# Optimization experiments

Hardware: AMD Instinct MI355X
Metric: run time of the kernel (lower is better)

Reference implementation:

```python
import jax, jax.numpy as jnp
import numpy as np

B, NW, NS, SL = 32, 500, 50, 40
EMB, HID, VOCAB, E = 300, 150, 50000, 563200
N = B * (NW + NS)
MAXPOS = 512


def _sinusoid(n_pos, d):
    pos = np.arange(n_pos)[:, None].astype(np.float64)
    i = np.arange(d)[None, :]
    ang = pos / np.power(10000.0, 2 * (i // 2) / d)
    tab = np.zeros((n_pos, d))
    tab[:, 0::2] = np.sin(ang[:, 0::2])
    tab[:, 1::2] = np.cos(ang[:, 1::2])
    tab[0] = 0.0  # padding_idx=0
    return jnp.asarray(tab, dtype=jnp.float32)

_POS_TAB = _sinusoid(MAXPOS + 1, EMB)


def setup_inputs():
    keys = iter(jax.random.split(jax.random.key(0), 48))
    def nrm(shape, s=0.05):
        return jax.random.normal(next(keys), shape, dtype=jnp.float32) * s
    inp = {}
    inp["x"] = jax.random.randint(next(keys), (B, NW), 0, VOCAB, dtype=jnp.int32)
    inp["sent_x"] = jax.random.randint(next(keys), (B, NS, SL), 0, VOCAB, dtype=jnp.int32)
    inp["edge_index"] = jax.random.randint(next(keys), (2, E), 0, N, dtype=jnp.int32)
    inp["embed_table"] = nrm((VOCAB, EMB)).at[0].set(0.0)  # padding_idx=0
    for h in range(2, 8):
        inp["conv_w%d" % h] = nrm((50, 1, h, EMB))
        inp["conv_b%d" % h] = nrm((50,))
    inp["cnn_proj_w"] = nrm((HID, EMB)); inp["cnn_proj_b"] = nrm((HID,))
    inp["lstm_w_ih_l0"] = nrm((2, 4 * HID, HID)); inp["lstm_w_hh_l0"] = nrm((2, 4 * HID, HID))
    inp["lstm_b_ih_l0"] = nrm((2, 4 * HID)); inp["lstm_b_hh_l0"] = nrm((2, 4 * HID))
    inp["lstm_w_ih_l1"] = nrm((2, 4 * HID, 2 * HID)); inp["lstm_w_hh_l1"] = nrm((2, 4 * HID, HID))
    inp["lstm_b_ih_l1"] = nrm((2, 4 * HID)); inp["lstm_b_hh_l1"] = nrm((2, 4 * HID))
    inp["lstm_proj_w"] = nrm((HID, 2 * HID)); inp["lstm_proj_b"] = nrm((HID,))
    inp["gc0_w"] = nrm((HID, EMB)); inp["gc0_b"] = nrm((HID,))
    inp["gc1_w"] = nrm((HID, HID)); inp["gc1_b"] = nrm((HID,))
    inp["gc2_w"] = nrm((HID, HID)); inp["gc2_b"] = nrm((HID,))
    return inp


def _forward(x, sent_x, edge_index, embed_table, conv_ws, conv_bs,
             cnn_proj_w, cnn_proj_b, w_ih0, w_hh0, b_ih0, b_hh0,
             w_ih1, w_hh1, b_ih1, b_hh1, lstm_proj_w, lstm_proj_b,
             gc0_w, gc0_b, gc1_w, gc1_b, gc2_w, gc2_b):
    Bsz, S, L = sent_x.shape
    Nn = Bsz * S
    emb_words = embed_table[x]                                   # [B, NW, EMB]
    tok = embed_table[sent_x].reshape(Nn, L, EMB)                # [Nn, L, EMB]
    sentlen = (sent_x != 0).sum(-1).reshape(Nn)                  # token count per sentence
    a = jnp.arange(L)
    input_pos = jnp.where(a[None, :] < sentlen[:, None], a[None, :] + 1, 0)
    enc = tok + _POS_TAB[input_pos]
    # CNN ngram features: conv heights 2..7, full-width kernels == windowed matmuls
    feats = []
    for w, b in zip(conv_ws, conv_bs):
        h = w.shape[2]
        acc = b + sum(jnp.einsum('nld,od->nlo', enc[:, k:L - h + 1 + k, :], w[:, 0, k, :]) for k in range(h))
        feats.append(jnp.max(jax.nn.relu(acc), axis=1))          # [Nn, 50]
    ngram = jnp.concatenate(feats, axis=1)                        # [Nn, 300]
    snode_pos = jnp.tile(jnp.arange(S), Bsz)
    cnn_feat = ((ngram + _POS_TAB[snode_pos]) @ cnn_proj_w.T + cnn_proj_b).reshape(Bsz, S, HID)
    glen = (sent_x[:, :, 0] != 0).sum(-1)                         # valid sentence count per graph

    def lstm_dir(xs, w_ih, w_hh, bias):
        def step(carry, xt):
            hh, cc = carry
            g = xt @ w_ih.T + hh @ w_hh.T + bias
            i, f, gg, o = jnp.split(g, 4, axis=-1)
            cc = jax.nn.sigmoid(f) * cc + jax.nn.sigmoid(i) * jnp.tanh(gg)
            hh = jax.nn.sigmoid(o) * jnp.tanh(cc)
            return (hh, cc), hh
        z = jnp.zeros((xs.shape[0], HID), xs.dtype)
        _, hs = jax.lax.scan(step, (z, z), jnp.swapaxes(xs, 0, 1))
        return jnp.swapaxes(hs, 0, 1)

    def rev_within(xs):
        # reverse only the first glen[b] steps (packed-sequence semantics)
        T = xs.shape[1]; t = jnp.arange(T)
        idx = jnp.where(t[None, :] < glen[:, None], glen[:, None] - 1 - t[None, :], t[None, :])
        return jnp.take_along_axis(xs, idx[:, :, None], axis=1)

    def bidir(xs, w_ih, w_hh, b_i, b_h):
        f = lstm_dir(xs, w_ih[0], w_hh[0], b_i[0] + b_h[0])
        r = rev_within(lstm_dir(rev_within(xs), w_ih[1], w_hh[1], b_i[1] + b_h[1]))
        return jnp.concatenate([f, r], axis=-1)

    h1 = bidir(cnn_feat, w_ih0, w_hh0, b_ih0, b_hh0)
    h2 = bidir(h1, w_ih1, w_hh1, b_ih1, b_hh1)
    mask = (jnp.arange(S)[None, :] < glen[:, None]).astype(h2.dtype)[:, :, None]
    lstm_feat = (h2 * mask) @ lstm_proj_w.T + lstm_proj_b
    sent_out = jnp.concatenate([cnn_feat, lstm_feat], axis=-1)    # [B, S, 300]
    nodes = jnp.concatenate([emb_words, sent_out], axis=1)        # [B, NW+S, 300]
    nodes = (nodes @ gc0_w.T + gc0_b).reshape(-1, HID)            # [N, 150]
    Nt = nodes.shape[0]
    loop = jnp.arange(Nt, dtype=edge_index.dtype)
    src = jnp.concatenate([edge_index[0], loop])                  # add self-loops
    dst = jnp.concatenate([edge_index[1], loop])
    deg = jax.ops.segment_sum(jnp.ones(src.shape[0], nodes.dtype), dst, num_segments=Nt)
    dis = jnp.where(deg > 0, jax.lax.rsqrt(deg), 0.0)
    norm = (dis[src] * dis[dst])[:, None]

    def gcn(xin, w, bias):
        xw = xin @ w.T
        return jax.ops.segment_sum(xw[src] * norm, dst, num_segments=Nt) + bias

    h = jax.nn.elu(gcn(nodes, gc1_w, gc1_b))
    # F.dropout with training=False -> identity
    return gcn(h, gc2_w, gc2_b), emb_words


def reference(x, sent_x, edge_index, embed_table, conv_w2, conv_b2, conv_w3, conv_b3,
              conv_w4, conv_b4, conv_w5, conv_b5, conv_w6, conv_b6, conv_w7, conv_b7,
              cnn_proj_w, cnn_proj_b, lstm_w_ih_l0, lstm_w_hh_l0, lstm_b_ih_l0, lstm_b_hh_l0,
              lstm_w_ih_l1, lstm_w_hh_l1, lstm_b_ih_l1, lstm_b_hh_l1, lstm_proj_w, lstm_proj_b,
              gc0_w, gc0_b, gc1_w, gc1_b, gc2_w, gc2_b):
    conv_ws = [conv_w2, conv_w3, conv_w4, conv_w5, conv_w6, conv_w7]
    conv_bs = [conv_b2, conv_b3, conv_b4, conv_b5, conv_b6, conv_b7]
    return _forward(x, sent_x, edge_index, embed_table, conv_ws, conv_bs,
                    cnn_proj_w, cnn_proj_b, lstm_w_ih_l0, lstm_w_hh_l0, lstm_b_ih_l0, lstm_b_hh_l0,
                    lstm_w_ih_l1, lstm_w_hh_l1, lstm_b_ih_l1, lstm_b_hh_l1, lstm_proj_w, lstm_proj_b,
                    gc0_w, gc0_b, gc1_w, gc1_b, gc2_w, gc2_b)
```

## Files before the change

kernel.cpp:

```cpp
#include <hip/hip_runtime.h>
#include <stdint.h>
#include <math.h>

#define EDGES 563200
#define NNODES 17600
#define OUT0SZ 2640000
#define MROWS 64000
#define MPAD  64016
#define KSTRIDE 2112

typedef _Float16 h2 __attribute__((ext_vector_type(2)));
typedef _Float16 h4 __attribute__((ext_vector_type(4)));
typedef _Float16 v8h __attribute__((ext_vector_type(8)));
typedef float v4f __attribute__((ext_vector_type(4)));

__device__ __forceinline__ float sigm(float x){ return 1.f / (1.f + expf(-x)); }

__device__ __forceinline__ float fdot2_(h2 a, h2 b, float c){
#if __has_builtin(__builtin_amdgcn_fdot2)
  return __builtin_amdgcn_fdot2(a, b, c, false);
#else
  return c + (float)a.x * (float)b.x + (float)a.y * (float)b.y;
#endif
}

__device__ __forceinline__ void stage16(const char* g, char* lds_base, int lane){
#if __has_builtin(__builtin_amdgcn_global_load_lds)
  __builtin_amdgcn_global_load_lds(
      (const __attribute__((address_space(1))) void*)g,
      (__attribute__((address_space(3))) void*)lds_base, 16, 0, 0);
#else
  uint4 v = *(const uint4*)g;
  *(uint4*)(lds_base + lane * 16) = v;
#endif
}

__global__ void gcnk_postab(float* __restrict__ pos){
  int idx = blockIdx.x * 256 + threadIdx.x;
  if (idx >= 513 * 300) return;
  int p = idx / 300, i = idx - p * 300;
  float v = 0.f;
  if (p != 0){
    double expo = (double)(2 * (i / 2)) / 300.0;
    double ang = (double)p / pow(10000.0, expo);
    v = (float)((i & 1) ? cos(ang) : sin(ang));
  }
  pos[idx] = v;
}

__global__ void gcnk_prep(const int* __restrict__ sx, int* __restrict__ sentlen,
                          int* __restrict__ glen){
  int tid = blockIdx.x * 256 + threadIdx.x;
  if (tid < 1600){
    int c = 0;
    for (int j = 0; j < 40; j++) c += (sx[tid * 40 + j] != 0);
    sentlen[tid] = c;
  } else if (tid < 1632){
    int b = tid - 1600, c = 0;
    for (int s = 0; s < 50; s++) c += (sx[b * 2000 + s * 40] != 0);
    glen[b] = c;
  }
}

__global__ void gcnk_rowmap(const int* __restrict__ glen, int* __restrict__ rowmap){
  int i = blockIdx.x * 256 + threadIdx.x;
  if (i >= 1600) return;
  int b = i / 50, t = i - b * 50, g = glen[b];
  rowmap[i] = b * 50 + ((t < g) ? (g - 1 - t) : t);
}

__global__ void gcnk_embw(const int* __restrict__ x, const float* __restrict__ tab,
                          float4* __restrict__ out){
  int idx = blockIdx.x * 256 + threadIdx.x;
  if (idx >= 16000 * 75) return;
  int row = idx / 75, q = idx - row * 75;
  const float4* t = (const float4*)tab;
  out[idx] = t[x[row] * 75 + q];
}

__global__ void gcnk_zeroi(unsigned int* __restrict__ p, int n){
  int i = blockIdx.x * 256 + threadIdx.x;
  if (i < n) p[i] = 0u;
}

__global__ void gcnk_ench(const int* __restrict__ sx, const float* __restrict__ tab,
                          const float* __restrict__ pos, const int* __restrict__ sentlen,
                          _Float16* __restrict__ ench){
  int idx = blockIdx.x * 256 + threadIdx.x;
  if (idx >= MPAD * 75) return;
  int row = idx / 75, q = idx - row * 75;
  int d = q * 4;
  h4 o; o[0] = (_Float16)0.f; o[1] = (_Float16)0.f; o[2] = (_Float16)0.f; o[3] = (_Float16)0.f;
  if (row < MROWS){
    int n = row / 40, l = row - n * 40;
    int tok = sx[n * 40 + l];
    int p = (l < sentlen[n]) ? (l + 1) : 0;
    float4 a = *(const float4*)(tab + (size_t)tok * 300 + d);
    float4 b = *(const float4*)(pos + (size_t)p * 300 + d);
    o[0] = (_Float16)(a.x + b.x); o[1] = (_Float16)(a.y + b.y);
    o[2] = (_Float16)(a.z + b.z); o[3] = (_Float16)(a.w + b.w);
  }
  *(h4*)(ench + (size_t)row * 300 + d) = o;
}

__global__ void gcnk_bpack(const float* w2, const float* w3, const float* w4,
                           const float* w5, const float* w6, const float* w7,
                           const float* c2, const float* c3, const float* c4,
                           const float* c5, const float* c6, const float* c7,
                           _Float16* __restrict__ Bp, float* __restrict__ bias_p){
  int idx = blockIdx.x * 256 + threadIdx.x;
  if (idx < 2 * 160 * KSTRIDE){
    int n = idx / KSTRIDE, kk = idx - n * KSTRIDE;
    int g = n / 160, c = n - g * 160;
    _Float16 v = (_Float16)0.f;
    if (c < 150){
      int H = 3 * g + 2 + c / 50, o = c % 50;
      if (kk < 300 * H){
        const float* w;
        switch (H){ case 2: w = w2; break; case 3: w = w3; break;
                    case 4: w = w4; break; case 5: w = w5; break;
                    case 6: w = w6; break; default: w = w7; break; }
        v = (_Float16)w[o * 300 * H + kk];
      }
    }
    Bp[idx] = v;
  }
  if (idx < 320){
    int g = idx / 160, c = idx - g * 160;
    float bv = 0.f;
    if (c < 150){
      int H = 3 * g + 2 + c / 50, o = c % 50;
      const float* cbp;
      switch (H){ case 2: cbp = c2; break; case 3: cbp = c3; break;
                  case 4: cbp = c4; break; case 5: cbp = c5; break;
                  case 6: cbp = c6; break; default: cbp = c7; break; }
      bv = cbp[o];
    }
    bias_p[idx] = bv;
  }
}

__global__ __launch_bounds__(256)
void gcnk_convmfma(const _Float16* __restrict__ A, const _Float16* __restrict__ Bp,
                   const float* __restrict__ bias_p, unsigned int* __restrict__ ngram_u){
  __shared__ __align__(1024) char smem[36864];
  _Float16* Asm = (_Float16*)smem;
  _Float16* Bsm = (_Float16*)(smem + 16384);
  float* Cs = (float*)smem;
  const int tid = threadIdx.x;
  const int m0 = blockIdx.x * 128;
  const int grp = blockIdx.y;
  const char* Abase = (const char*)A;
  const char* Bbase = (const char*)(Bp + (size_t)grp * 160 * KSTRIDE);
  const int kmax = grp ? 2112 : 1216;
  const int w = tid >> 6, lane = tid & 63;
  const int wm = (w >> 1) * 64, wn = (w & 1) * 80;
  const int fm = lane & 15, fq = lane >> 4;
  const int lrow = lane >> 3;
  const int loff = (((lane & 7) ^ lrow) << 4);

  v4f acc[4][5] = {};

  for (int kc = 0; kc < kmax; kc += 64){
    #pragma unroll
    for (int ii = 0; ii < 4; ii++){
      int i = w * 4 + ii;
      const char* g = Abase + (size_t)(m0 + i * 8 + lrow) * 600 + kc * 2 + loff;
      stage16(g, (char*)Asm + i * 1024, lane);
    }
    #pragma unroll
    for (int jj = 0; jj < 5; jj++){
      int j = w * 5 + jj;
      const char* g = Bbase + (size_t)(j * 8 + lrow) * (KSTRIDE * 2) + kc * 2 + loff;
      stage16(g, (char*)Bsm + j * 1024, lane);
    }
    __syncthreads();
    #pragma unroll
    for (int ks = 0; ks < 2; ks++){
      const int axor = (ks * 64 + fq * 16) ^ ((fm & 7) << 4);
      v8h af[4], bf[5];
      #pragma unroll
      for (int mt = 0; mt < 4; mt++)
        af[mt] = *(const v8h*)((const char*)Asm + (wm + mt * 16 + fm) * 128 + axor);
      #pragma unroll
      for (int nt = 0; nt < 5; nt++)
        bf[nt] = *(const v8h*)((const char*)Bsm + (wn + nt * 16 + fm) * 128 + axor);
      #pragma unroll
      for (int mt = 0; mt < 4; mt++)
        #pragma unroll
        for (int nt = 0; nt < 5; nt++)
          acc[mt][nt] = __builtin_amdgcn_mfma_f32_16x16x32_f16(af[mt], bf[nt], acc[mt][nt], 0, 0, 0);
    }
    __syncthreads();
  }

  for (int p = 0; p < 5; p++){
    __syncthreads();
    #pragma unroll
    for (int nt = 0; nt < 5; nt++){
      int cstart = wn + nt * 16;
      if ((cstart >> 5) == p){
        int co = cstart - p * 32 + fm;
        #pragma unroll
        for (int mt = 0; mt < 4; mt++)
          #pragma unroll
          for (int r = 0; r < 4; r++)
            Cs[(wm + mt * 16 + fq * 4 + r) * 33 + co] = acc[mt][nt][r];
      }
    }
    __syncthreads();
    if (tid < 128){
      int cl = tid & 31, si = tid >> 5;
      int col = p * 32 + cl;
      if (col < 150){
        int H = 3 * grp + 2 + col / 50, lh = 41 - H;
        int sent = m0 / 40 + si;
        if (sent < 1600){
          int rlo = sent * 40; if (rlo < m0) rlo = m0;
          int rhi = sent * 40 + lh; if (rhi > m0 + 128) rhi = m0 + 128;
          if (rlo < rhi){
            float bv = bias_p[grp * 160 + col];
            float vmax = 0.f;
            for (int r = rlo; r < rhi; r++){
              float v = Cs[(r - m0) * 33 + cl] + bv;
              vmax = fmaxf(vmax, v);
            }
            atomicMax(ngram_u + sent * 300 + grp * 150 + col, __float_as_uint(vmax));
          }
        }
      }
    }
  }
}

__global__ void gcnk_addpos(float* __restrict__ ngram, const float* __restrict__ pos){
  int idx = blockIdx.x * 256 + threadIdx.x;
  if (idx >= 1600 * 300) return;
  int row = idx / 300, d = idx - row * 300;
  ngram[idx] += pos[(row % 50) * 300 + d];
}

template<int BM, int BN, int WMT, int WNT, int OUTH>
__global__ __launch_bounds__(256)
void gcnk_mgemm(const float* __restrict__ A, const float* __restrict__ Wt,
                const float* __restrict__ b1, const float* __restrict__ b2,
                void* __restrict__ Cv, int M, int N, int K){
  __shared__ __align__(16) _Float16 As[BM * 40];
  __shared__ __align__(16) _Float16 Bs[BN * 40];
  const int tid = threadIdx.x;
  const int m0 = blockIdx.x * BM, n0 = blockIdx.y * BN;
  const int w = tid >> 6, lane = tid & 63;
  const int wm = (w >> 1) * (WMT * 16), wn = (w & 1) * (WNT * 16);
  const int fm = lane & 15, fq = lane >> 4;
  v4f acc[WMT][WNT] = {};
  const int nch = (K + 31) >> 5;
  for (int ch = 0; ch < nch; ch++){
    int kc = ch * 32;
    #pragma unroll
    for (int j = 0; j < BM / 64; j++){
      int u = tid + 256 * j;
      int row = u >> 2, cb = (u & 3) * 8;
      int gm = m0 + row, gk = kc + cb;
      v8h vv;
      if (gm < M && gk + 8 <= K){
        const float* p = A + (size_t)gm * K + gk;
        #pragma unroll
        for (int e = 0; e < 8; e++) vv[e] = (_Float16)p[e];
      } else {
        #pragma unroll
        for (int e = 0; e < 8; e++)
          vv[e] = (gm < M && gk + e < K) ? (_Float16)A[(size_t)gm * K + gk + e] : (_Float16)0.f;
      }
      *(v8h*)(As + row * 40 + cb) = vv;
    }
    {
      int row = tid >> 2, cb = (tid & 3) * 8;
      int gn = n0 + row, gk = kc + cb;
      v8h vv;
      if (gn < N && gk + 8 <= K){
        const float* p = Wt + (size_t)gn * K + gk;
        #pragma unroll
        for (int e = 0; e < 8; e++) vv[e] = (_Float16)p[e];
      } else {
        #pragma unroll
        for (int e = 0; e < 8; e++)
          vv[e] = (gn < N && gk + e < K) ? (_Float16)Wt[(size_t)gn * K + gk + e] : (_Float16)0.f;
      }
      *(v8h*)(Bs + row * 40 + cb) = vv;
    }
    __syncthreads();
    v8h af[WMT], bf[WNT];
    #pragma unroll
    for (int mt = 0; mt < WMT; mt++)
      af[mt] = *(const v8h*)(As + (wm + mt * 16 + fm) * 40 + fq * 8);
    #pragma unroll
    for (int nt = 0; nt < WNT; nt++)
      bf[nt] = *(const v8h*)(Bs + (wn + nt * 16 + fm) * 40 + fq * 8);
    #pragma unroll
    for (int mt = 0; mt < WMT; mt++)
      #pragma unroll
      for (int nt = 0; nt < WNT; nt++)
        acc[mt][nt] = __builtin_amdgcn_mfma_f32_16x16x32_f16(af[mt], bf[nt], acc[mt][nt], 0, 0, 0);
    __syncthreads();
  }
  #pragma unroll
  for (int nt = 0; nt < WNT; nt++){
    int gn = n0 + wn + nt * 16 + fm;
    if (gn >= N) continue;
    float badd = (b1 ? b1[gn] : 0.f) + (b2 ? b2[gn] : 0.f);
    #pragma unroll
    for (int mt = 0; mt < WMT; mt++)
      #pragma unroll
      for (int r = 0; r < 4; r++){
        int gm = m0 + wm + mt * 16 + fq * 4 + r;
        if (gm < M){
          float val = acc[mt][nt][r] + badd;
          if (OUTH) ((_Float16*)Cv)[(size_t)gm * 160 + gn] = (_Float16)val;
          else      ((float*)Cv)[(size_t)gm * N + gn] = val;
        }
      }
  }
}

__global__ void gcnk_permute150(float* __restrict__ dst, const float* __restrict__ src,
                                const int* __restrict__ map){
  int idx = blockIdx.x * 256 + threadIdx.x;
  if (idx >= 1600 * 150) return;
  int row = idx / 150, d = idx - row * 150;
  dst[idx] = src[map[row] * 150 + d];
}

__global__ void gcnk_concat(float* __restrict__ dst, const float* __restrict__ A,
                            const float* __restrict__ Bs, const int* __restrict__ mapA,
                            const int* __restrict__ mapB, const int* __restrict__ glen,
                            int usemask){
  int idx = blockIdx.x * 256 + threadIdx.x;
  if (idx >= 1600 * 300) return;
  int row = idx / 300, d = idx - row * 300;
  int b = row / 50, t = row - b * 50;
  float v;
  if (d < 150){ int r = mapA ? mapA[row] : row; v = A[r * 150 + d]; }
  else        { int r = mapB ? mapB[row] : row; v = Bs[r * 150 + d - 150]; }
  if (usemask && t >= glen[b]) v = 0.f;
  dst[idx] = v;
}

__global__ void gcnk_whhpack(const float* __restrict__ whh, _Float16* __restrict__ wpad){
  int idx = blockIdx.x * 256 + threadIdx.x;
  if (idx >= 1200 * 152) return;
  int row = idx / 152, col = idx - row * 152;
  wpad[idx] = (col < 150) ? (_Float16)whh[row * 150 + col] : (_Float16)0.f;
}

__global__ __launch_bounds__(640)
void gcnk_lstm(const float* __restrict__ xf, const float* __restrict__ xr,
               const _Float16* __restrict__ wpad, float* __restrict__ fo,
               float* __restrict__ ro){
  int b = blockIdx.x >> 1, dir = blockIdx.x & 1;
  const float* xih = dir ? xr : xf;
  float* out = dir ? ro : fo;
  __shared__ __align__(16) _Float16 hh[160];
  __shared__ float gates[600];
  const int tid = threadIdx.x;

  h2 w[76];
  if (tid < 600){
    const h2* wrow = (const h2*)(wpad + ((size_t)dir * 600 + tid) * 152);
    #pragma unroll
    for (int j = 0; j < 76; j++) w[j] = wrow[j];
  }
  for (int u = tid; u < 160; u += 640) hh[u] = (_Float16)0.f;
  float creg = 0.f;
  __syncthreads();

  for (int t = 0; t < 50; t++){
    if (tid < 600){
      float acc = xih[(b * 50 + t) * 600 + tid];
      float a0 = 0.f, a1 = 0.f, a2 = 0.f, a3 = 0.f;
      #pragma unroll
      for (int j = 0; j < 19; j++){
        union { float4 f; h2 h[4]; } u;
        u.f = *(const float4*)(hh + j * 8);
        a0 = fdot2_(w[4 * j + 0], u.h[0], a0);
        a1 = fdot2_(w[4 * j + 1], u.h[1], a1);
        a2 = fdot2_(w[4 * j + 2], u.h[2], a2);
        a3 = fdot2_(w[4 * j + 3], u.h[3], a3);
      }
      gates[tid] = acc + ((a0 + a1) + (a2 + a3));
    }
    __syncthreads();
    if (tid < 150){
      float ig = sigm(gates[tid]);
      float fg = sigm(gates[150 + tid]);
      float gg = tanhf(gates[300 + tid]);
      float og = sigm(gates[450 + tid]);
      creg = fg * creg + ig * gg;
      float hn = og * tanhf(creg);
      hh[tid] = (_Float16)hn;
      out[(b * 50 + t) * 150 + tid] = hn;
    }
    __syncthreads();
  }
}

__global__ void gcnk_nodes_in(const int* __restrict__ x, const float* __restrict__ tab,
                              const float* __restrict__ cnnf, const float* __restrict__ lstmf,
                              float* __restrict__ out){
  int idx = blockIdx.x * 256 + threadIdx.x;
  if (idx >= NNODES * 300) return;
  int nrow = idx / 300, d = idx - nrow * 300;
  int b = nrow / 550, j = nrow - b * 550;
  float v;
  if (j < 500) v = tab[x[b * 500 + j] * 300 + d];
  else {
    int r = b * 50 + (j - 500);
    v = (d < 150) ? cnnf[r * 150 + d] : lstmf[r * 150 + d - 150];
  }
  out[idx] = v;
}

__global__ void gcnk_hist(const int* __restrict__ ei, int* __restrict__ ecnt){
  int e = blockIdx.x * 256 + threadIdx.x;
  if (e < EDGES) atomicAdd(&ecnt[ei[EDGES + e]], 1);
}

__global__ __launch_bounds__(1024)
void gcnk_scan(const int* __restrict__ ecnt, int* __restrict__ eoff,
               int* __restrict__ ecur){
  __shared__ int wsum[16];
  int tid = threadIdx.x;
  int base = tid * 18;
  int pre[18];
  int s = 0;
  #pragma unroll
  for (int i = 0; i < 18; i++){
    int idx = base + i;
    int c = (idx < NNODES) ? ecnt[idx] : 0;
    pre[i] = s; s += c;
  }
  int lane = tid & 63, wid = tid >> 6;
  int run = s;
  #pragma unroll
  for (int off = 1; off < 64; off <<= 1){
    int y = __shfl_up(run, off, 64);
    if (lane >= off) run += y;
  }
  if (lane == 63) wsum[wid] = run;
  __syncthreads();
  if (tid == 0){
    int a = 0;
    #pragma unroll
    for (int i = 0; i < 16; i++){ int t2 = wsum[i]; wsum[i] = a; a += t2; }
  }
  __syncthreads();
  int excl = wsum[wid] + run - s;
  #pragma unroll
  for (int i = 0; i < 18; i++){
    int idx = base + i;
    if (idx < NNODES){
      int e = excl + pre[i];
      eoff[idx] = e; ecur[idx] = e;
    }
  }
}

__global__ void gcnk_scatter(const int* __restrict__ ei, int* __restrict__ ecur,
                             int* __restrict__ esrc){
  int e = blockIdx.x * 256 + threadIdx.x;
  if (e < EDGES){
    int d = ei[EDGES + e];
    int p = atomicAdd(&ecur[d], 1);
    esrc[p] = ei[e];
  }
}

__global__ void gcnk_dis2(const int* __restrict__ ecnt, float* __restrict__ dis){
  int i = blockIdx.x * 256 + threadIdx.x;
  if (i < NNODES) dis[i] = rsqrtf((float)(ecnt[i] + 1));
}

__global__ __launch_bounds__(128)
void gcnk_aggcsr_h(const int* __restrict__ eoff, const int* __restrict__ ecnt,
                   const int* __restrict__ esrc, const float* __restrict__ dis,
                   const _Float16* __restrict__ xw, const float* __restrict__ bias,
                   float* __restrict__ out, int doelu){
  int d = blockIdx.x, t = threadIdx.x;
  float dd = dis[d];
  bool act = t < 75;
  float ax = 0.f, ay = 0.f;
  if (act){
    h2 v = *(const h2*)(xw + (size_t)d * 160 + 2 * t);
    ax = (float)v[0] * dd; ay = (float)v[1] * dd;
  }
  int beg = eoff[d], end = beg + ecnt[d];
  for (int j = beg; j < end; j++){
    int s = esrc[j];
    float ds_ = dis[s];
    if (act){
      h2 v = *(const h2*)(xw + (size_t)s * 160 + 2 * t);
      ax += (float)v[0] * ds_; ay += (float)v[1] * ds_;
    }
  }
  if (act){
    float o0 = ax * dd + bias[2 * t];
    float o1 = ay * dd + bias[2 * t + 1];
    if (doelu){
      o0 = (o0 > 0.f) ? o0 : expm1f(o0);
      o1 = (o1 > 0.f) ? o1 : expm1f(o1);
    }
    *(float2*)(out + (size_t)d * 150 + 2 * t) = make_float2(o0, o1);
  }
}

extern "C" void kernel_launch(void* const* d_in, const int* in_sizes, int n_in,
                              void* d_out, int out_size, void* d_ws, size_t ws_size,
                              hipStream_t stream){
  (void)in_sizes; (void)n_in; (void)out_size; (void)ws_size;

  char* wsb = (char*)d_ws;
  size_t off = 0;
  auto alloc = [&](size_t bytes) -> void* {
    void* p = wsb + off;
    off = (off + bytes + 255) & ~(size_t)255;
    return p;
  };
  float* pos_tab  = (float*)alloc(513 * 300 * 4);
  int*   sentlen  = (int*)alloc(1600 * 4);
  int*   glen     = (int*)alloc(32 * 4);
  int*   rowmap   = (int*)alloc(1600 * 4);
  float* ngram    = (float*)alloc(1600 * 300 * 4);
  float* cnn_feat = (float*)alloc(1600 * 150 * 4);
  float* cnn_rev  = (float*)alloc(1600 * 150 * 4);
  float* xih_f    = (float*)alloc(1600 * 600 * 4);
  float* xih_r    = (float*)alloc(1600 * 600 * 4);
  float* f0       = (float*)alloc(1600 * 150 * 4);
  float* r0       = (float*)alloc(1600 * 150 * 4);
  float* f1       = (float*)alloc(1600 * 150 * 4);
  float* r1       = (float*)alloc(1600 * 150 * 4);
  float* h1       = (float*)alloc(1600 * 300 * 4);
  float* h1rev    = (float*)alloc(1600 * 300 * 4);
  float* hm       = (float*)alloc(1600 * 300 * 4);
  float* lstm_ft  = (float*)alloc(1600 * 150 * 4);
  float* nodes_in = (float*)alloc((size_t)NNODES * 300 * 4);
  float* nodes    = (float*)alloc((size_t)NNODES * 150 * 4);
  float* dis      = (float*)alloc(NNODES * 4);
  _Float16* xwh   = (_Float16*)alloc((size_t)NNODES * 160 * 2);
  _Float16* ench  = (_Float16*)alloc((size_t)MPAD * 300 * 2);
  _Float16* Bp    = (_Float16*)alloc((size_t)2 * 160 * KSTRIDE * 2);
  float* bias_p   = (float*)alloc(320 * 4);
  _Float16* wpad0 = (_Float16*)alloc(1200 * 152 * 2);
  _Float16* wpad1 = (_Float16*)alloc(1200 * 152 * 2);
  int*   ecnt     = (int*)alloc(NNODES * 4);
  int*   eoff     = (int*)alloc(NNODES * 4);
  int*   ecur     = (int*)alloc(NNODES * 4);
  int*   esrc     = (int*)alloc(EDGES * 4);

  const int*   x   = (const int*)d_in[0];
  const int*   sx  = (const int*)d_in[1];
  const int*   ei  = (const int*)d_in[2];
  const float* tab = (const float*)d_in[3];
  const float *cw[6], *cb[6];
  for (int h = 0; h < 6; h++){ cw[h] = (const float*)d_in[4 + 2 * h]; cb[h] = (const float*)d_in[5 + 2 * h]; }
  const float* cnnw = (const float*)d_in[16]; const float* cnnb = (const float*)d_in[17];
  const float* wih0 = (const float*)d_in[18]; const float* whh0 = (const float*)d_in[19];
  const float* bih0 = (const float*)d_in[20]; const float* bhh0 = (const float*)d_in[21];
  const float* wih1 = (const float*)d_in[22]; const float* whh1 = (const float*)d_in[23];
  const float* bih1 = (const float*)d_in[24]; const float* bhh1 = (const float*)d_in[25];
  const float* lpw  = (const float*)d_in[26]; const float* lpb  = (const float*)d_in[27];
  const float* g0w  = (const float*)d_in[28]; const float* g0b  = (const float*)d_in[29];
  const float* g1w  = (const float*)d_in[30]; const float* g1b  = (const float*)d_in[31];
  const float* g2w  = (const float*)d_in[32]; const float* g2b  = (const float*)d_in[33];

  float* out0 = (float*)d_out;
  float4* out1 = (float4*)((float*)d_out + OUT0SZ);

  auto mgemmL = [&](const float* A, const float* W, const float* b1, const float* b2,
                    void* C, int M, int N, int K){
    dim3 g((M + 127) / 128, (N + 63) / 64);
    gcnk_mgemm<128, 64, 4, 2, 0><<<g, 256, 0, stream>>>(A, W, b1, b2, C, M, N, K);
  };
  auto mgemmLH = [&](const float* A, const float* W, void* C, int M, int N, int K){
    dim3 g((M + 127) / 128, (N + 63) / 64);
    gcnk_mgemm<128, 64, 4, 2, 1><<<g, 256, 0, stream>>>(A, W, nullptr, nullptr, C, M, N, K);
  };
  auto mgemmS = [&](const float* A, const float* W, const float* b1, const float* b2,
                    void* C, int M, int N, int K){
    dim3 g((M + 63) / 64, (N + 63) / 64);
    gcnk_mgemm<64, 64, 2, 2, 0><<<g, 256, 0, stream>>>(A, W, b1, b2, C, M, N, K);
  };

  gcnk_postab<<<602, 256, 0, stream>>>(pos_tab);
  gcnk_prep<<<7, 256, 0, stream>>>(sx, sentlen, glen);
  gcnk_rowmap<<<7, 256, 0, stream>>>(glen, rowmap);
  gcnk_embw<<<4688, 256, 0, stream>>>(x, tab, out1);

  gcnk_zeroi<<<1875, 256, 0, stream>>>((unsigned int*)ngram, 1600 * 300);
  gcnk_ench<<<(MPAD * 75 + 255) / 256, 256, 0, stream>>>(sx, tab, pos_tab, sentlen, ench);
  gcnk_bpack<<<(2 * 160 * KSTRIDE + 255) / 256, 256, 0, stream>>>(
      cw[0], cw[1], cw[2], cw[3], cw[4], cw[5],
      cb[0], cb[1], cb[2], cb[3], cb[4], cb[5], Bp, bias_p);
  gcnk_whhpack<<<713, 256, 0, stream>>>(whh0, wpad0);
  gcnk_whhpack<<<713, 256, 0, stream>>>(whh1, wpad1);
  {
    dim3 g(500, 2);
    gcnk_convmfma<<<g, 256, 0, stream>>>(ench, Bp, bias_p, (unsigned int*)ngram);
  }
  gcnk_addpos<<<1875, 256, 0, stream>>>(ngram, pos_tab);
  mgemmS(ngram, cnnw, cnnb, nullptr, cnn_feat, 1600, 150, 300);

  gcnk_permute150<<<938, 256, 0, stream>>>(cnn_rev, cnn_feat, rowmap);
  mgemmS(cnn_feat, wih0,             bih0,       bhh0,       xih_f, 1600, 600, 150);
  mgemmS(cnn_rev,  wih0 + 600 * 150, bih0 + 600, bhh0 + 600, xih_r, 1600, 600, 150);
  gcnk_lstm<<<64, 640, 0, stream>>>(xih_f, xih_r, wpad0, f0, r0);

  gcnk_concat<<<1875, 256, 0, stream>>>(h1,    f0, r0, nullptr, rowmap, glen, 0);
  gcnk_concat<<<1875, 256, 0, stream>>>(h1rev, f0, r0, rowmap, nullptr, glen, 0);
  mgemmS(h1,    wih1,             bih1,       bhh1,       xih_f, 1600, 600, 300);
  mgemmS(h1rev, wih1 + 600 * 300, bih1 + 600, bhh1 + 600, xih_r, 1600, 600, 300);
  gcnk_lstm<<<64, 640, 0, stream>>>(xih_f, xih_r, wpad1, f1, r1);

  gcnk_concat<<<1875, 256, 0, stream>>>(hm, f1, r1, nullptr, rowmap, glen, 1);
  mgemmS(hm, lpw, lpb, nullptr, lstm_ft, 1600, 150, 300);

  gcnk_nodes_in<<<20625, 256, 0, stream>>>(x, tab, cnn_feat, lstm_ft, nodes_in);
  mgemmL(nodes_in, g0w, g0b, nullptr, nodes, NNODES, 150, 300);

  gcnk_zeroi<<<69, 256, 0, stream>>>((unsigned int*)ecnt, NNODES);
  gcnk_hist<<<2200, 256, 0, stream>>>(ei, ecnt);
  gcnk_scan<<<1, 1024, 0, stream>>>(ecnt, eoff, ecur);
  gcnk_scatter<<<2200, 256, 0, stream>>>(ei, ecur, esrc);
  gcnk_dis2<<<69, 256, 0, stream>>>(ecnt, dis);

  mgemmLH(nodes, g1w, xwh, NNODES, 150, 150);
  gcnk_aggcsr_h<<<NNODES, 128, 0, stream>>>(eoff, ecnt, esrc, dis, xwh, g1b, nodes, 1);

  mgemmLH(nodes, g2w, xwh, NNODES, 150, 150);
  gcnk_aggcsr_h<<<NNODES, 128, 0, stream>>>(eoff, ecnt, esrc, dis, xwh, g2b, out0, 0);
}
```

Measured before the change: 829.0 us.

## Fuse gather, concat and mask staging into the MFMA GEMM operand loads

Removes the separate permute, concat and nodes_in gather kernels by folding row remapping, bidirectional concatenation, length masking and embedding lookup straight into the A-tile loads of the GEMMs. Two new GEMM kernels (a generic 1600-row fused variant and a node-feature variant with 128-row tiles) replace the earlier templated calls for these stages. The aim is to cut launches and the global round trips through intermediate buffers, especially the 17600x300 nodes_in tensor. In exchange the A loads become scalar, indirect, per-element gathers with branching, which may load less efficiently than the old contiguous layout.

```diff
diff --git a/kernel.cpp b/kernel.cpp
--- a/kernel.cpp
+++ b/kernel.cpp
@@ -322,27 +322,218 @@
   }
 }
 
-__global__ void gcnk_permute150(float* __restrict__ dst, const float* __restrict__ src,
-                                const int* __restrict__ map){
-  int idx = blockIdx.x * 256 + threadIdx.x;
-  if (idx >= 1600 * 150) return;
-  int row = idx / 150, d = idx - row * 150;
-  dst[idx] = src[map[row] * 150 + d];
-}
-
-__global__ void gcnk_concat(float* __restrict__ dst, const float* __restrict__ A,
-                            const float* __restrict__ Bs, const int* __restrict__ mapA,
-                            const int* __restrict__ mapB, const int* __restrict__ glen,
-                            int usemask){
-  int idx = blockIdx.x * 256 + threadIdx.x;
-  if (idx >= 1600 * 300) return;
-  int row = idx / 300, d = idx - row * 300;
-  int b = row / 50, t = row - b * 50;
-  float v;
-  if (d < 150){ int r = mapA ? mapA[row] : row; v = A[r * 150 + d]; }
-  else        { int r = mapB ? mapB[row] : row; v = Bs[r * 150 + d - 150]; }
-  if (usemask && t >= glen[b]) v = 0.f;
-  dst[idx] = v;
+__global__ __launch_bounds__(256)
+void gcnk_mgemmF(const float* __restrict__ A1, const int* __restrict__ mapA,
+                 const float* __restrict__ A2, const int* __restrict__ mapB,
+                 const int* __restrict__ glen, int usemask,
+                 const float* __restrict__ Wt, const float* __restrict__ b1,
+                 const float* __restrict__ b2, float* __restrict__ C,
+                 int M, int N, int K){
+  const int BM = 64, WMT = 2, WNT = 2;
+  __shared__ __align__(16) _Float16 As[BM * 40];
+  __shared__ __align__(16) _Float16 Bs[64 * 40];
+  const int tid = threadIdx.x;
+  const int m0 = blockIdx.x * BM, n0 = blockIdx.y * 64;
+  const int w = tid >> 6, lane = tid & 63;
+  const int wm = (w >> 1) * (WMT * 16), wn = (w & 1) * (WNT * 16);
+  const int fm = lane & 15, fq = lane >> 4;
+  v4f acc[WMT][WNT] = {};
+  const int nch = (K + 31) >> 5;
+  for (int ch = 0; ch < nch; ch++){
+    int kc = ch * 32;
+    {
+      int row = tid >> 2, cb = (tid & 3) * 8;
+      int gm = m0 + row, gk = kc + cb;
+      v8h vv;
+      bool ok = (gm < M);
+      if (ok && usemask){
+        int b = gm / 50;
+        if (gm - b * 50 >= glen[b]) ok = false;
+      }
+      if (!ok){
+        #pragma unroll
+        for (int e = 0; e < 8; e++) vv[e] = (_Float16)0.f;
+      } else if (!A2){
+        int r = mapA ? mapA[gm] : gm;
+        const float* base = A1 + (size_t)r * K;
+        if (gk + 8 <= K){
+          #pragma unroll
+          for (int e = 0; e < 8; e++) vv[e] = (_Float16)base[gk + e];
+        } else {
+          #pragma unroll
+          for (int e = 0; e < 8; e++)
+            vv[e] = (gk + e < K) ? (_Float16)base[gk + e] : (_Float16)0.f;
+        }
+      } else {
+        int rA = mapA ? mapA[gm] : gm;
+        int rB = mapB ? mapB[gm] : gm;
+        const float* pa = A1 + (size_t)rA * 150;
+        const float* pb = A2 + (size_t)rB * 150;
+        if (gk + 8 <= 150){
+          #pragma unroll
+          for (int e = 0; e < 8; e++) vv[e] = (_Float16)pa[gk + e];
+        } else if (gk >= 150){
+          #pragma unroll
+          for (int e = 0; e < 8; e++)
+            vv[e] = (gk + e < K) ? (_Float16)pb[gk + e - 150] : (_Float16)0.f;
+        } else {
+          #pragma unroll
+          for (int e = 0; e < 8; e++){
+            int c = gk + e;
+            vv[e] = (c < 150) ? (_Float16)pa[c]
+                  : ((c < K) ? (_Float16)pb[c - 150] : (_Float16)0.f);
+          }
+        }
+      }
+      *(v8h*)(As + row * 40 + cb) = vv;
+    }
+    {
+      int row = tid >> 2, cb = (tid & 3) * 8;
+      int gn = n0 + row, gk = kc + cb;
+      v8h vv;
+      if (gn < N && gk + 8 <= K){
+        const float* p = Wt + (size_t)gn * K + gk;
+        #pragma unroll
+        for (int e = 0; e < 8; e++) vv[e] = (_Float16)p[e];
+      } else {
+        #pragma unroll
+        for (int e = 0; e < 8; e++)
+          vv[e] = (gn < N && gk + e < K) ? (_Float16)Wt[(size_t)gn * K + gk + e] : (_Float16)0.f;
+      }
+      *(v8h*)(Bs + row * 40 + cb) = vv;
+    }
+    __syncthreads();
+    v8h af[WMT], bf[WNT];
+    #pragma unroll
+    for (int mt = 0; mt < WMT; mt++)
+      af[mt] = *(const v8h*)(As + (wm + mt * 16 + fm) * 40 + fq * 8);
+    #pragma unroll
+    for (int nt = 0; nt < WNT; nt++)
+      bf[nt] = *(const v8h*)(Bs + (wn + nt * 16 + fm) * 40 + fq * 8);
+    #pragma unroll
+    for (int mt = 0; mt < WMT; mt++)
+      #pragma unroll
+      for (int nt = 0; nt < WNT; nt++)
+        acc[mt][nt] = __builtin_amdgcn_mfma_f32_16x16x32_f16(af[mt], bf[nt], acc[mt][nt], 0, 0, 0);
+    __syncthreads();
+  }
+  #pragma unroll
+  for (int nt = 0; nt < WNT; nt++){
+    int gn = n0 + wn + nt * 16 + fm;
+    if (gn >= N) continue;
+    float badd = (b1 ? b1[gn] : 0.f) + (b2 ? b2[gn] : 0.f);
+    #pragma unroll
+    for (int mt = 0; mt < WMT; mt++)
+      #pragma unroll
+      for (int r = 0; r < 4; r++){
+        int gm = m0 + wm + mt * 16 + fq * 4 + r;
+        if (gm < M) C[(size_t)gm * N + gn] = acc[mt][nt][r] + badd;
+      }
+  }
+}
+
+__global__ __launch_bounds__(256)
+void gcnk_mgemmN(const int* __restrict__ x, const float* __restrict__ tab,
+                 const float* __restrict__ cnnf, const float* __restrict__ lstmf,
+                 const float* __restrict__ Wt, const float* __restrict__ b1,
+                 float* __restrict__ C, int N){
+  const int M = NNODES, K = 300;
+  __shared__ __align__(16) _Float16 As[128 * 40];
+  __shared__ __align__(16) _Float16 Bs[64 * 40];
+  const int tid = threadIdx.x;
+  const int m0 = blockIdx.x * 128, n0 = blockIdx.y * 64;
+  const int w = tid >> 6, lane = tid & 63;
+  const int wm = (w >> 1) * 64, wn = (w & 1) * 32;
+  const int fm = lane & 15, fq = lane >> 4;
+  v4f acc[4][2] = {};
+  for (int ch = 0; ch < 10; ch++){
+    int kc = ch * 32;
+    #pragma unroll
+    for (int j = 0; j < 2; j++){
+      int u = tid + 256 * j;
+      int row = u >> 2, cb = (u & 3) * 8;
+      int gm = m0 + row, gk = kc + cb;
+      v8h vv;
+      if (gm < M){
+        int b = gm / 550, jj = gm - b * 550;
+        if (jj < 500){
+          const float* p = tab + (size_t)x[b * 500 + jj] * 300;
+          if (gk + 8 <= 300){
+            #pragma unroll
+            for (int e = 0; e < 8; e++) vv[e] = (_Float16)p[gk + e];
+          } else {
+            #pragma unroll
+            for (int e = 0; e < 8; e++)
+              vv[e] = (gk + e < 300) ? (_Float16)p[gk + e] : (_Float16)0.f;
+          }
+        } else {
+          int r = b * 50 + (jj - 500);
+          const float* pa = cnnf + (size_t)r * 150;
+          const float* pb = lstmf + (size_t)r * 150;
+          if (gk + 8 <= 150){
+            #pragma unroll
+            for (int e = 0; e < 8; e++) vv[e] = (_Float16)pa[gk + e];
+          } else if (gk >= 150 && gk + 8 <= 300){
+            #pragma unroll
+            for (int e = 0; e < 8; e++) vv[e] = (_Float16)pb[gk + e - 150];
+          } else {
+            #pragma unroll
+            for (int e = 0; e < 8; e++){
+              int c = gk + e;
+              vv[e] = (c < 150) ? (_Float16)pa[c]
+                    : ((c < 300) ? (_Float16)pb[c - 150] : (_Float16)0.f);
+            }
+          }
+        }
+      } else {
+        #pragma unroll
+        for (int e = 0; e < 8; e++) vv[e] = (_Float16)0.f;
+      }
+      *(v8h*)(As + row * 40 + cb) = vv;
+    }
+    {
+      int row = tid >> 2, cb = (tid & 3) * 8;
+      int gn = n0 + row, gk = kc + cb;
+      v8h vv;
+      if (gn < N && gk + 8 <= K){
+        const float* p = Wt + (size_t)gn * K + gk;
+        #pragma unroll
+        for (int e = 0; e < 8; e++) vv[e] = (_Float16)p[e];
+      } else {
+        #pragma unroll
+        for (int e = 0; e < 8; e++)
+          vv[e] = (gn < N && gk + e < K) ? (_Float16)Wt[(size_t)gn * K + gk + e] : (_Float16)0.f;
+      }
+      *(v8h*)(Bs + row * 40 + cb) = vv;
+    }
+    __syncthreads();
+    v8h af[4], bf[2];
+    #pragma unroll
+    for (int mt = 0; mt < 4; mt++)
+      af[mt] = *(const v8h*)(As + (wm + mt * 16 + fm) * 40 + fq * 8);
+    #pragma unroll
+    for (int nt = 0; nt < 2; nt++)
+      bf[nt] = *(const v8h*)(Bs + (wn + nt * 16 + fm) * 40 + fq * 8);
+    #pragma unroll
+    for (int mt = 0; mt < 4; mt++)
+      #pragma unroll
+      for (int nt = 0; nt < 2; nt++)
+        acc[mt][nt] = __builtin_amdgcn_mfma_f32_16x16x32_f16(af[mt], bf[nt], acc[mt][nt], 0, 0, 0);
+    __syncthreads();
+  }
+  #pragma unroll
+  for (int nt = 0; nt < 2; nt++){
+    int gn = n0 + wn + nt * 16 + fm;
+    if (gn >= N) continue;
+    float badd = b1[gn];
+    #pragma unroll
+    for (int mt = 0; mt < 4; mt++)
+      #pragma unroll
+      for (int r = 0; r < 4; r++){
+        int gm = m0 + wm + mt * 16 + fq * 4 + r;
+        if (gm < M) C[(size_t)gm * N + gn] = acc[mt][nt][r] + badd;
+      }
+  }
 }
 
 __global__ void gcnk_whhpack(const float* __restrict__ whh, _Float16* __restrict__ wpad){
@@ -401,22 +592,6 @@
     }
     __syncthreads();
   }
-}
-
-__global__ void gcnk_nodes_in(const int* __restrict__ x, const float* __restrict__ tab,
-                              const float* __restrict__ cnnf, const float* __restrict__ lstmf,
-                              float* __restrict__ out){
-  int idx = blockIdx.x * 256 + threadIdx.x;
-  if (idx >= NNODES * 300) return;
-  int nrow = idx / 300, d = idx - nrow * 300;
-  int b = nrow / 550, j = nrow - b * 550;
-  float v;
-  if (j < 500) v = tab[x[b * 500 + j] * 300 + d];
-  else {
-    int r = b * 50 + (j - 500);
-    v = (d < 150) ? cnnf[r * 150 + d] : lstmf[r * 150 + d - 150];
-  }
-  out[idx] = v;
 }
 
 __global__ void gcnk_hist(const int* __restrict__ ei, int* __restrict__ ecnt){
@@ -530,18 +705,13 @@
   int*   rowmap   = (int*)alloc(1600 * 4);
   float* ngram    = (float*)alloc(1600 * 300 * 4);
   float* cnn_feat = (float*)alloc(1600 * 150 * 4);
-  float* cnn_rev  = (float*)alloc(1600 * 150 * 4);
   float* xih_f    = (float*)alloc(1600 * 600 * 4);
   float* xih_r    = (float*)alloc(1600 * 600 * 4);
   float* f0       = (float*)alloc(1600 * 150 * 4);
   float* r0       = (float*)alloc(1600 * 150 * 4);
   float* f1       = (float*)alloc(1600 * 150 * 4);
   float* r1       = (float*)alloc(1600 * 150 * 4);
-  float* h1       = (float*)alloc(1600 * 300 * 4);
-  float* h1rev    = (float*)alloc(1600 * 300 * 4);
-  float* hm       = (float*)alloc(1600 * 300 * 4);
   float* lstm_ft  = (float*)alloc(1600 * 150 * 4);
-  float* nodes_in = (float*)alloc((size_t)NNODES * 300 * 4);
   float* nodes    = (float*)alloc((size_t)NNODES * 150 * 4);
   float* dis      = (float*)alloc(NNODES * 4);
   _Float16* xwh   = (_Float16*)alloc((size_t)NNODES * 160 * 2);
@@ -574,19 +744,15 @@
   float* out0 = (float*)d_out;
   float4* out1 = (float4*)((float*)d_out + OUT0SZ);
 
-  auto mgemmL = [&](const float* A, const float* W, const float* b1, const float* b2,
-                    void* C, int M, int N, int K){
-    dim3 g((M + 127) / 128, (N + 63) / 64);
-    gcnk_mgemm<128, 64, 4, 2, 0><<<g, 256, 0, stream>>>(A, W, b1, b2, C, M, N, K);
-  };
   auto mgemmLH = [&](const float* A, const float* W, void* C, int M, int N, int K){
     dim3 g((M + 127) / 128, (N + 63) / 64);
     gcnk_mgemm<128, 64, 4, 2, 1><<<g, 256, 0, stream>>>(A, W, nullptr, nullptr, C, M, N, K);
   };
-  auto mgemmS = [&](const float* A, const float* W, const float* b1, const float* b2,
-                    void* C, int M, int N, int K){
-    dim3 g((M + 63) / 64, (N + 63) / 64);
-    gcnk_mgemm<64, 64, 2, 2, 0><<<g, 256, 0, stream>>>(A, W, b1, b2, C, M, N, K);
+  auto mgemmF = [&](const float* A1, const int* mapA, const float* A2, const int* mapB,
+                    const int* gl, int um, const float* W, const float* b1,
+                    const float* b2, float* C, int N, int K){
+    dim3 g(25, (N + 63) / 64);
+    gcnk_mgemmF<<<g, 256, 0, stream>>>(A1, mapA, A2, mapB, gl, um, W, b1, b2, C, 1600, N, K);
   };
 
   gcnk_postab<<<602, 256, 0, stream>>>(pos_tab);
@@ -606,24 +772,26 @@
     gcnk_convmfma<<<g, 256, 0, stream>>>(ench, Bp, bias_p, (unsigned int*)ngram);
   }
   gcnk_addpos<<<1875, 256, 0, stream>>>(ngram, pos_tab);
-  mgemmS(ngram, cnnw, cnnb, nullptr, cnn_feat, 1600, 150, 300);
-
-  gcnk_permute150<<<938, 256, 0, stream>>>(cnn_rev, cnn_feat, rowmap);
-  mgemmS(cnn_feat, wih0,             bih0,       bhh0,       xih_f, 1600, 600, 150);
-  mgemmS(cnn_rev,  wih0 + 600 * 150, bih0 + 600, bhh0 + 600, xih_r, 1600, 600, 150);
+  mgemmF(ngram, nullptr, nullptr, nullptr, nullptr, 0, cnnw, cnnb, nullptr, cnn_feat, 150, 300);
+
+  mgemmF(cnn_feat, nullptr, nullptr, nullptr, nullptr, 0,
+         wih0,             bih0,       bhh0,       xih_f, 600, 150);
+  mgemmF(cnn_feat, rowmap,  nullptr, nullptr, nullptr, 0,
+         wih0 + 600 * 150, bih0 + 600, bhh0 + 600, xih_r, 600, 150);
   gcnk_lstm<<<64, 640, 0, stream>>>(xih_f, xih_r, wpad0, f0, r0);
 
-  gcnk_concat<<<1875, 256, 0, stream>>>(h1,    f0, r0, nullptr, rowmap, glen, 0);
-  gcnk_concat<<<1875, 256, 0, stream>>>(h1rev, f0, r0, rowmap, nullptr, glen, 0);
-  mgemmS(h1,    wih1,             bih1,       bhh1,       xih_f, 1600, 600, 300);
-  mgemmS(h1rev, wih1 + 600 * 300, bih1 + 600, bhh1 + 600, xih_r, 1600, 600, 300);
+  mgemmF(f0, nullptr, r0, rowmap, nullptr, 0,
+         wih1,             bih1,       bhh1,       xih_f, 600, 300);
+  mgemmF(f0, rowmap, r0, nullptr, nullptr, 0,
+         wih1 + 600 * 300, bih1 + 600, bhh1 + 600, xih_r, 600, 300);
   gcnk_lstm<<<64, 640, 0, stream>>>(xih_f, xih_r, wpad1, f1, r1);
 
-  gcnk_concat<<<1875, 256, 0, stream>>>(hm, f1, r1, nullptr, rowmap, glen, 1);
-  mgemmS(hm, lpw, lpb, nullptr, lstm_ft, 1600, 150, 300);
-
-  gcnk_nodes_in<<<20625, 256, 0, stream>>>(x, tab, cnn_feat, lstm_ft, nodes_in);
-  mgemmL(nodes_in, g0w, g0b, nullptr, nodes, NNODES, 150, 300);
+  mgemmF(f1, nullptr, r1, rowmap, glen, 1, lpw, lpb, nullptr, lstm_ft, 150, 300);
+
+  {
+    dim3 g(138, 3);
+    gcnk_mgemmN<<<g, 256, 0, stream>>>(x, tab, cnn_feat, lstm_ft, g0w, g0b, nodes, 150);
+  }
 
   gcnk_zeroi<<<69, 256, 0, stream>>>((unsigned int*)ecnt, NNODES);
   gcnk_hist<<<2200, 256, 0, stream>>>(ei, ecnt);
```

New measurement: 847.2 us. 1.02x slower.
